# Kernel optimization log

Measured on AMD Instinct MI355X. Metric: run time of the kernel, lower is better.

Reference implementation:

```python
import jax, jax.numpy as jnp
import numpy as np

ANGLE_BITS = 3          # TurboQuantConfig.angle_bits default
LEVELS = 2 ** ANGLE_BITS
PI = np.pi


def _angle_ranges(d_minus_1, dtype):
    # hyperspherical coords: first d-2 angles in [0, pi], last angle in [0, 2*pi)
    return jnp.concatenate([
        jnp.full((d_minus_1 - 1,), PI, dtype),
        jnp.full((1,), 2.0 * PI, dtype),
    ])


def polar_compress(x):
    """x: [..., d] -> (r [...,1], theta_indices int32 [..., d-1])."""
    # suffix norms s_i = ||x[i:]|| via reversed cumsum of squares
    suffix = jnp.sqrt(jnp.cumsum((x * x)[..., ::-1], axis=-1)[..., ::-1])
    r = suffix[..., :1]
    cos_t = jnp.clip(x[..., :-1] / jnp.maximum(suffix[..., :-1], 1e-12), -1.0, 1.0)
    theta = jnp.arccos(cos_t)                      # [..., d-1], in [0, pi]
    # last angle carries the sign of x[..., -1]: map to [0, 2*pi)
    last = jnp.where(x[..., -1:] < 0, 2.0 * PI - theta[..., -1:], theta[..., -1:])
    theta = jnp.concatenate([theta[..., :-1], last], axis=-1)
    ranges = _angle_ranges(theta.shape[-1], theta.dtype)
    idx = jnp.round(theta / ranges * (LEVELS - 1)).astype(jnp.int32)
    return r, idx


def polar_decompress(r, idx):
    """(r [...,1], idx [..., d-1]) -> x_hat [..., d] via trig products."""
    d1 = idx.shape[-1]
    ranges = _angle_ranges(d1, r.dtype)
    theta = idx.astype(r.dtype) / (LEVELS - 1) * ranges
    sinp = jnp.cumprod(jnp.sin(theta), axis=-1)                 # [..., d-1]
    prods = jnp.concatenate([jnp.ones_like(r), sinp], axis=-1)  # [..., d]
    coss = jnp.concatenate([jnp.cos(theta), jnp.ones_like(r)], axis=-1)
    return r * prods * coss


def setup_inputs() -> dict:
    key = jax.random.key(0)
    kq, kk, kv, kn = jax.random.split(key, 4)
    B, H, T, k, d = 1, 32, 8192, 16, 128
    return {
        "queries": jax.random.normal(kq, (B, H, k, d), jnp.float32),
        "keys": jax.random.normal(kk, (B, H, T, d), jnp.float32),
        "values": jax.random.normal(kv, (B, H, T, d), jnp.float32),
        # faithful stand-in for `torch.randn_like(scores) * 0.01` QJL correction,
        # materialized deterministically as an input
        "qjl_noise": jax.random.normal(kn, (B, H, k, T), jnp.float32) * 0.01,
    }


def reference(queries, keys, values, qjl_noise):
    d = queries.shape[-1]
    # compress_kv_cache: polar angle quantization of keys and values
    r_k, idx_k = polar_compress(keys)
    r_v, idx_v = polar_compress(values)
    # compute_attention_with_compressed_kv: decompress-then-attend
    keys_polar = polar_decompress(r_k, idx_k)      # [B,H,T,d]
    values_polar = polar_decompress(r_v, idx_v)    # [B,H,T,d]
    scores = jnp.einsum('bhkd,bhtd->bhkt', queries, keys_polar) / jnp.sqrt(
        jnp.asarray(d, queries.dtype))
    scores = scores + qjl_noise
    attn = jax.nn.softmax(scores, axis=-1)
    return jnp.einsum('bhkt,bhtd->bhkd', attn, values_polar)
```

## Files before the change

### kernel.cpp

```cpp
#include <hip/hip_runtime.h>
#include <math.h>

typedef __attribute__((ext_vector_type(8))) short bf16x8;
typedef __attribute__((ext_vector_type(4))) float f32x4;
typedef __attribute__((ext_vector_type(2))) float f32x2;

#define HEADS 32
#define SEQT  8192
#define DIM   128
#define NQ    16
#define BPH   64
#define BTOK  128
#define WTOK  32
#define CHK   16
#define NPART BPH
#define PSTR  132
#define QSCALE 0.08838834764831845f

#define OFF_QS    0
#define OFF_PS    4096
#define OFF_RAW   8192
#define OFF_KS    24576
#define OFF_ML    0
#define OFF_MERGE 8192
#define LDS_BYTES 40960

#define W1SQ 0.9504844339512096f
#define W2SQ 0.6112604669781572f
#define W3SQ 0.1882550990706332f
#define S1C  0.4338837391175581f
#define S2C  0.7818314824680298f
#define S3C  0.9749279121818236f
#define C1C  0.9009688679024191f
#define C2C  0.6234898018587336f
#define C3C  0.2225209339563144f
#define B1SQ 0.8117449009293667f
#define B2SQ 0.0495155660487913f
#define B3SQ 0.3887395330218429f

#define DPP_QP_XOR1 0xB1
#define DPP_QP_XOR2 0x4E
#define DPP_QP_SHL1 0x39
#define DPP_QP_SHR1 0x90
#define DPP_QP_SHR2 0x44
#define DPP_QP_BC0  0x00
#define DPP_QP_BC3  0xFF
#define DPP_HALF_MIRR 0x141
#define DPP_MIRR      0x140

#define WAITV asm volatile("s_waitcnt vmcnt(0)" ::: "memory")

template <int CTRL>
__device__ __forceinline__ float dpp0(float v) {
  return __int_as_float(__builtin_amdgcn_update_dpp(
      0, __float_as_int(v), CTRL, 0xF, 0xF, true));
}
__device__ __forceinline__ float rmax16(float v) {
  v = fmaxf(v, dpp0<DPP_QP_XOR1>(v));
  v = fmaxf(v, dpp0<DPP_QP_XOR2>(v));
  v = fmaxf(v, dpp0<DPP_HALF_MIRR>(v));
  v = fmaxf(v, dpp0<DPP_MIRR>(v));
  return v;
}
__device__ __forceinline__ float rsum16(float v) {
  v += dpp0<DPP_QP_XOR1>(v);
  v += dpp0<DPP_QP_XOR2>(v);
  v += dpp0<DPP_HALF_MIRR>(v);
  v += dpp0<DPP_MIRR>(v);
  return v;
}
__device__ __forceinline__ float rdlane(float v, int l) {
  return __int_as_float(__builtin_amdgcn_readlane(__float_as_int(v), l));
}
__device__ __forceinline__ unsigned short f2bf(float f) {
  unsigned u = __float_as_uint(f);
  u += 0x7FFFu + ((u >> 16) & 1u);
  return (unsigned short)(u >> 16);
}
__device__ __forceinline__ unsigned cvtpk(float lo, float hi) {
  unsigned r;
  asm("v_cvt_pk_bf16_f32 %0, %1, %2" : "=v"(r) : "v"(lo), "v"(hi));
  return r;
}

__device__ __forceinline__ void stage8(const float* __restrict__ g, char* lds, int lane) {
  const int h2 = lane >> 5;
  const int qs = (lane >> 3) & 3;
  const int js = lane & 7;
#pragma unroll
  for (int i = 0; i < 4; ++i) {
    const int t = 2 * i + h2;
    const int sb = js ^ t;
    __builtin_amdgcn_global_load_lds(
        (const float*)(g + (size_t)t * DIM + qs * 32 + sb * 4),
        (float*)(lds + i * 1024), 16, 0, 0);
  }
}

template <bool KOUT>
__device__ __forceinline__ void decomp8(
    const float* rawW, int lane,
    unsigned short* KsW, float* VsW, int q8,
    const float* nextsrc, char* rawBytes)
{
  const int tloc = lane >> 3;
  const int o    = lane & 7;

  float x[16];
#pragma unroll
  for (int j = 0; j < 4; ++j) {
    const int s = ((o >> 1) << 3) | ((((o & 1) << 2) | j) ^ tloc);
    const float4 v = *(const float4*)(rawW + tloc * 128 + 4 * s);
    x[4*j+0] = v.x; x[4*j+1] = v.y; x[4*j+2] = v.z; x[4*j+3] = v.w;
  }
  asm volatile("s_waitcnt lgkmcnt(0)" ::: "memory");
  __builtin_amdgcn_sched_barrier(0);
  if (nextsrc) stage8(nextsrc, rawBytes, lane);
  __builtin_amdgcn_sched_barrier(0);

  float qa0 = 0.f, qa1 = 0.f;
#pragma unroll
  for (int i = 0; i < 16; i += 2) {
    qa0 = fmaf(x[i], x[i], qa0);
    qa1 = fmaf(x[i+1], x[i+1], qa1);
  }
  const float qs = qa0 + qa1;
  const float a1 = dpp0<DPP_QP_SHL1>(qs);
  const float t1 = qs + (((lane & 3) == 3) ? 0.f : a1);
  const float b1 = dpp0<DPP_QP_XOR2>(t1);
  const float t2 = t1 + (((lane & 3) < 2) ? b1 : 0.f);
  const float qt = dpp0<DPP_QP_BC0>(t2);
  const float ot = dpp0<DPP_HALF_MIRR>(qt);
  const float total = qt + ot;
  const float S = t2 + ((o < 4) ? ot : 0.f);

  const float r = sqrtf(total);

  float run = S, psin = 1.f, run14 = 0.f;
  float sv[16], cv[16];
#pragma unroll
  for (int i = 0; i < 16; ++i) {
    const float u = x[i] * x[i];
    if (i == 14) run14 = run;
    const bool lo2 = u < W2SQ * run;
    const float thr = lo2 ? W3SQ : W1SQ;
    const bool bx = u < thr * run;
    const float ssin = lo2 ? (bx ? S3C : S2C) : (bx ? S1C : 0.f);
    float scos = lo2 ? (bx ? C3C : C2C) : (bx ? C1C : 1.f);
    scos = copysignf(scos, x[i]);
    sv[i] = ssin; cv[i] = scos;
    psin *= ssin;
    run -= u;
  }
  const float p1 = dpp0<DPP_QP_SHR1>(psin);
  const float e1 = psin * (((lane & 3) == 0) ? 1.f : p1);
  const float p2 = dpp0<DPP_QP_SHR2>(e1);
  const float e2 = e1 * (((lane & 3) < 2) ? 1.f : p2);
  const float pq = dpp0<DPP_QP_BC3>(e2);
  const float po = dpp0<DPP_HALF_MIRR>(pq);
  const float e3 = e2 * ((o >= 4) ? po : 1.f);
  const float sh = dpp0<DPP_QP_SHR1>(e3);
  const float E = ((lane & 3) == 0) ? ((o < 4) ? 1.f : po) : sh;

  float rcum = r * E;
  const int T = q8 * 8 + tloc;
#pragma unroll
  for (int g = 0; g < 2; ++g) {
    float outv[8];
    float rc14 = rcum;
#pragma unroll
    for (int k = 0; k < 8; ++k) {
      const int i = 8 * g + k;
      if (i == 14) rc14 = rcum;
      outv[k] = rcum * cv[i];
      rcum *= sv[i];
    }
    if (g == 1) {
      const float u14 = x[14] * x[14];
      const bool neg = x[14] < 0.f;
      const bool cc1 = u14 < B1SQ * run14;
      const bool cc2 = u14 < B2SQ * run14;
      const bool cc3 = u14 > B3SQ * run14;
      const float cpos = cc2 ? -C3C : (cc1 ? C2C : 1.f);
      const float spos = cc2 ? S3C : (cc1 ? S2C : 0.f);
      const float cneg = cc3 ? -C1C : -C3C;
      const float sneg = cc3 ? S1C : S3C;
      const float cB = neg ? cneg : cpos;
      float sB = neg ? sneg : spos;
      sB = copysignf(sB, x[15]);
      const bool o7 = (o == 7);
      outv[6] = o7 ? rc14 * cB : outv[6];
      outv[7] = o7 ? rc14 * sB : outv[7];
    }
    if (KOUT) {
      uint4 w;
      w.x = cvtpk(outv[0], outv[1]);
      w.y = cvtpk(outv[2], outv[3]);
      w.z = cvtpk(outv[4], outv[5]);
      w.w = cvtpk(outv[6], outv[7]);
      *(uint4*)&KsW[T * 128 + ((o * 16 + 8 * g) ^ (tloc << 3))] = w;
    } else {
      const int f0 = (o * 16 + 8 * g) ^ (tloc << 2);
      *(float4*)&VsW[tloc * 128 + f0]       = make_float4(outv[0], outv[1], outv[2], outv[3]);
      *(float4*)&VsW[tloc * 128 + (f0 ^ 4)] = make_float4(outv[4], outv[5], outv[6], outv[7]);
    }
  }
}

__global__ __launch_bounds__(256, 2)
void attn_partial(const float* __restrict__ Q, const float* __restrict__ K,
                  const float* __restrict__ V, const float* __restrict__ noise,
                  float* __restrict__ part) {
  __shared__ __align__(16) char RAW[LDS_BYTES];
  unsigned short* Qs = (unsigned short*)(RAW + OFF_QS);
  float*          Ps = (float*)(RAW + OFF_PS);
  float2*         Ml = (float2*)(RAW + OFF_ML);

  const int tid  = threadIdx.x;
  const int lane = tid & 63;
  const int wv   = tid >> 6;
  const int h    = blockIdx.x / BPH;
  const int bh   = blockIdx.x % BPH;
  const int r16  = lane & 15, G = lane >> 4;

  char* rawB = RAW + OFF_RAW + wv * 4096;
  const float* rawW = (const float*)rawB;
  unsigned short* KsW = (unsigned short*)(RAW + OFF_KS + wv * 4096);
  float* VsW = (float*)KsW;
  float* myP = Ps + wv * (CHK * NQ);

  const size_t hoff = (size_t)h * SEQT * DIM;
  const int t0 = bh * BTOK + wv * WTOK;
  const float* Kg = K + hoff + (size_t)t0 * DIM;
  const float* Vg = V + hoff + (size_t)t0 * DIM;

  stage8(Kg, rawB, lane);
  {
    const float* Qh = Q + (size_t)h * NQ * DIM;
    for (int i = tid; i < NQ * DIM; i += 256)
      Qs[i] = f2bf(Qh[i] * QSCALE);
  }
  __syncthreads();

  bf16x8 qa[4];
#pragma unroll
  for (int c = 0; c < 4; ++c)
    qa[c] = *(const bf16x8*)&Qs[r16 * 128 + c * 32 + G * 8];

  f32x2 acc[NQ];
#pragma unroll
  for (int qq = 0; qq < NQ; ++qq) acc[qq] = (f32x2){0.f, 0.f};
  float m_r[4] = {-INFINITY, -INFINITY, -INFINITY, -INFINITY};
  float l_r[4] = {0.f, 0.f, 0.f, 0.f};

  const float* nh = noise + (size_t)h * NQ * SEQT + t0 + r16;

#pragma unroll 1
  for (int ch = 0; ch < 2; ++ch) {
    const float* KgC = Kg + ch * 2048;
    const float* VgC = Vg + ch * 2048;

    WAITV;
    decomp8<true>(rawW, lane, KsW, VsW, 0, KgC + 1024, rawB);
    WAITV;
    decomp8<true>(rawW, lane, KsW, VsW, 1, VgC, rawB);

    f32x4 d0 = {0.f, 0.f, 0.f, 0.f};
#pragma unroll
    for (int c = 0; c < 4; ++c) {
      bf16x8 b0 = *(const bf16x8*)&KsW[r16 * 128 + ((c * 32 + G * 8) ^ ((r16 & 7) << 3))];
      d0 = __builtin_amdgcn_mfma_f32_16x16x32_bf16(qa[c], b0, d0, 0, 0, 0);
    }
    const float* nt = nh + ch * CHK;
    float s0_[4];
#pragma unroll
    for (int rr = 0; rr < 4; ++rr)
      s0_[rr] = d0[rr] + nt[(size_t)(4 * G + rr) * SEQT];
    float al_r[4];
#pragma unroll
    for (int rr = 0; rr < 4; ++rr) {
      float mt = rmax16(s0_[rr]);
      float mn = fmaxf(m_r[rr], mt);
      al_r[rr] = __expf(m_r[rr] - mn);
      m_r[rr] = mn;
    }
    float p0[4];
#pragma unroll
    for (int rr = 0; rr < 4; ++rr) {
      p0[rr] = __expf(s0_[rr] - m_r[rr]);
      l_r[rr] = l_r[rr] * al_r[rr] + rsum16(p0[rr]);
    }
    *(float4*)&myP[r16 * NQ + 4 * G] = make_float4(p0[0], p0[1], p0[2], p0[3]);
#pragma unroll
    for (int qq = 0; qq < NQ; ++qq) {
      float alq = rdlane(al_r[qq & 3], (qq >> 2) << 4);
      acc[qq] *= (f32x2){alq, alq};
    }

#pragma unroll 1
    for (int sc = 0; sc < 2; ++sc) {
      const float* nxt = (sc == 0) ? (VgC + 1024)
                                   : ((ch == 0) ? (KgC + 2048) : nullptr);
      WAITV;
      decomp8<false>(rawW, lane, KsW, VsW, 0, nxt, rawB);
#pragma unroll 2
      for (int tt = 0; tt < 8; ++tt) {
        float2 vh = *(const float2*)&VsW[tt * 128 + ((2 * lane) ^ (tt << 2))];
        f32x2 vh2 = {vh.x, vh.y};
        const float* pv = &myP[(sc * 8 + tt) * NQ];
        float4 pa = ((const float4*)pv)[0];
        float4 pb = ((const float4*)pv)[1];
        float4 pc = ((const float4*)pv)[2];
        float4 pd = ((const float4*)pv)[3];
        float pq[NQ] = {pa.x, pa.y, pa.z, pa.w, pb.x, pb.y, pb.z, pb.w,
                        pc.x, pc.y, pc.z, pc.w, pd.x, pd.y, pd.z, pd.w};
#pragma unroll
        for (int qq = 0; qq < NQ; ++qq)
          acc[qq] = __builtin_elementwise_fma((f32x2){pq[qq], pq[qq]}, vh2, acc[qq]);
      }
    }
  }

  if (r16 == 0) {
#pragma unroll
    for (int rr = 0; rr < 4; ++rr)
      Ml[wv * NQ + 4 * G + rr] = make_float2(m_r[rr], l_r[rr]);
  }
  __syncthreads();
#pragma unroll
  for (int qq = 0; qq < NQ; ++qq) {
    float2 e0 = Ml[0 * NQ + qq], e1 = Ml[1 * NQ + qq];
    float2 e2 = Ml[2 * NQ + qq], e3 = Ml[3 * NQ + qq];
    float Mq = fmaxf(fmaxf(e0.x, e1.x), fmaxf(e2.x, e3.x));
    float own = (wv == 0) ? e0.x : ((wv == 1) ? e1.x : ((wv == 2) ? e2.x : e3.x));
    float al = __expf(own - Mq);
    acc[qq] *= (f32x2){al, al};
  }
  float* buf = (float*)(RAW + OFF_MERGE);
  if (wv >= 2) {
#pragma unroll
    for (int qq = 0; qq < NQ; ++qq)
      *(float2*)&buf[(wv - 2) * 2048 + qq * 128 + 2 * lane] =
          make_float2(acc[qq].x, acc[qq].y);
  }
  __syncthreads();
  if (wv < 2) {
#pragma unroll
    for (int qq = 0; qq < NQ; ++qq) {
      float2 t = *(const float2*)&buf[wv * 2048 + qq * 128 + 2 * lane];
      acc[qq] += (f32x2){t.x, t.y};
    }
  }
  __syncthreads();
  if (wv == 1) {
#pragma unroll
    for (int qq = 0; qq < NQ; ++qq)
      *(float2*)&buf[qq * 128 + 2 * lane] = make_float2(acc[qq].x, acc[qq].y);
  }
  __syncthreads();
  if (wv == 0) {
    float* P = part + ((size_t)h * NPART + bh) * (NQ * PSTR);
#pragma unroll
    for (int qq = 0; qq < NQ; ++qq) {
      float2 t = *(const float2*)&buf[qq * 128 + 2 * lane];
      *(float2*)&P[qq * PSTR + 4 + 2 * lane] =
          make_float2(acc[qq].x + t.x, acc[qq].y + t.y);
      float2 e0 = Ml[0 * NQ + qq], e1 = Ml[1 * NQ + qq];
      float2 e2 = Ml[2 * NQ + qq], e3 = Ml[3 * NQ + qq];
      float Mq = fmaxf(fmaxf(e0.x, e1.x), fmaxf(e2.x, e3.x));
      float Lq = e0.y * __expf(e0.x - Mq) + e1.y * __expf(e1.x - Mq) +
                 e2.y * __expf(e2.x - Mq) + e3.y * __expf(e3.x - Mq);
      if (lane == 0) *(float2*)&P[qq * PSTR] = make_float2(Mq, Lq);
    }
  }
}

__global__ __launch_bounds__(128)
void attn_reduce(const float* __restrict__ part, float* __restrict__ out) {
  __shared__ float wgt[NPART];
  __shared__ float Lsh;
  const int tid = threadIdx.x;
  const int h = blockIdx.x >> 4;
  const int q = blockIdx.x & 15;
  const float* P = part + (size_t)h * NPART * NQ * PSTR;
  if (tid < NPART) {
    float2 ml = *(const float2*)&P[((size_t)tid * NQ + q) * PSTR];
    float M = ml.x;
#pragma unroll
    for (int off = 1; off < 64; off <<= 1)
      M = fmaxf(M, __shfl_xor(M, off, 64));
    float w = __expf(ml.x - M);
    wgt[tid] = w;
    float L = ml.y * w;
#pragma unroll
    for (int off = 1; off < 64; off <<= 1)
      L += __shfl_xor(L, off, 64);
    if (tid == 0) Lsh = L;
  }
  __syncthreads();
  const float* A = P + (size_t)q * PSTR + 4 + tid;
  float o = 0.f;
#pragma unroll 8
  for (int c = 0; c < NPART; ++c)
    o = fmaf(wgt[c], A[(size_t)c * NQ * PSTR], o);
  out[((size_t)h * NQ + q) * DIM + tid] = o * (1.0f / Lsh);
}

extern "C" void kernel_launch(void* const* d_in, const int* in_sizes, int n_in,
                              void* d_out, int out_size, void* d_ws, size_t ws_size,
                              hipStream_t stream) {
  (void)in_sizes; (void)n_in; (void)out_size; (void)ws_size;
  const float* Q = (const float*)d_in[0];
  const float* K = (const float*)d_in[1];
  const float* V = (const float*)d_in[2];
  const float* noise = (const float*)d_in[3];
  float* part = (float*)d_ws;
  attn_partial<<<dim3(HEADS * BPH), dim3(256), 0, stream>>>(Q, K, V, noise, part);
  attn_reduce<<<dim3(HEADS * NQ), dim3(128), 0, stream>>>(part, (float*)d_out);
}
```

Before: 307.0 us.

## Load raw K/V tiles into registers instead of staging through LDS

Replaces the global_load_lds staging of raw K/V rows, and the swizzled LDS reads that followed, with direct float4 global loads into registers. Double-buffered register arrays (xa/xb) prefetch the next 8-token tile while the current one is decompressed. This drops 16 KB of LDS per block and removes the explicit vmcnt waits and LDS round trips. The cost is 32 more live VGPRs under launch_bounds(256,2), which could cause spills or leave the compiler waiting on loads at first use.

```diff
diff --git a/kernel.cpp b/kernel.cpp
--- a/kernel.cpp
+++ b/kernel.cpp
@@ -19,11 +19,10 @@
 
 #define OFF_QS    0
 #define OFF_PS    4096
-#define OFF_RAW   8192
-#define OFF_KS    24576
+#define OFF_KS    8192
 #define OFF_ML    0
 #define OFF_MERGE 8192
-#define LDS_BYTES 40960
+#define LDS_BYTES 24576
 
 #define W1SQ 0.9504844339512096f
 #define W2SQ 0.6112604669781572f
@@ -48,8 +47,6 @@
 #define DPP_HALF_MIRR 0x141
 #define DPP_MIRR      0x140
 
-#define WAITV asm volatile("s_waitcnt vmcnt(0)" ::: "memory")
-
 template <int CTRL>
 __device__ __forceinline__ float dpp0(float v) {
   return __int_as_float(__builtin_amdgcn_update_dpp(
@@ -83,40 +80,24 @@
   return r;
 }
 
-__device__ __forceinline__ void stage8(const float* __restrict__ g, char* lds, int lane) {
-  const int h2 = lane >> 5;
-  const int qs = (lane >> 3) & 3;
-  const int js = lane & 7;
-#pragma unroll
-  for (int i = 0; i < 4; ++i) {
-    const int t = 2 * i + h2;
-    const int sb = js ^ t;
-    __builtin_amdgcn_global_load_lds(
-        (const float*)(g + (size_t)t * DIM + qs * 32 + sb * 4),
-        (float*)(lds + i * 1024), 16, 0, 0);
-  }
+__device__ __forceinline__ void loadx(float x[16], const float* __restrict__ g, int lane) {
+  const int tloc = lane >> 3;
+  const int o    = lane & 7;
+  const float4* p = (const float4*)(g + tloc * DIM + o * 16);
+  const float4 a = p[0], b = p[1], c = p[2], d = p[3];
+  x[0]=a.x;  x[1]=a.y;  x[2]=a.z;  x[3]=a.w;
+  x[4]=b.x;  x[5]=b.y;  x[6]=b.z;  x[7]=b.w;
+  x[8]=c.x;  x[9]=c.y;  x[10]=c.z; x[11]=c.w;
+  x[12]=d.x; x[13]=d.y; x[14]=d.z; x[15]=d.w;
 }
 
 template <bool KOUT>
 __device__ __forceinline__ void decomp8(
-    const float* rawW, int lane,
-    unsigned short* KsW, float* VsW, int q8,
-    const float* nextsrc, char* rawBytes)
+    const float (&x)[16], int lane,
+    unsigned short* KsW, float* VsW, int q8)
 {
   const int tloc = lane >> 3;
   const int o    = lane & 7;
-
-  float x[16];
-#pragma unroll
-  for (int j = 0; j < 4; ++j) {
-    const int s = ((o >> 1) << 3) | ((((o & 1) << 2) | j) ^ tloc);
-    const float4 v = *(const float4*)(rawW + tloc * 128 + 4 * s);
-    x[4*j+0] = v.x; x[4*j+1] = v.y; x[4*j+2] = v.z; x[4*j+3] = v.w;
-  }
-  asm volatile("s_waitcnt lgkmcnt(0)" ::: "memory");
-  __builtin_amdgcn_sched_barrier(0);
-  if (nextsrc) stage8(nextsrc, rawBytes, lane);
-  __builtin_amdgcn_sched_barrier(0);
 
   float qa0 = 0.f, qa1 = 0.f;
 #pragma unroll
@@ -223,8 +204,6 @@
   const int bh   = blockIdx.x % BPH;
   const int r16  = lane & 15, G = lane >> 4;
 
-  char* rawB = RAW + OFF_RAW + wv * 4096;
-  const float* rawW = (const float*)rawB;
   unsigned short* KsW = (unsigned short*)(RAW + OFF_KS + wv * 4096);
   float* VsW = (float*)KsW;
   float* myP = Ps + wv * (CHK * NQ);
@@ -234,7 +213,8 @@
   const float* Kg = K + hoff + (size_t)t0 * DIM;
   const float* Vg = V + hoff + (size_t)t0 * DIM;
 
-  stage8(Kg, rawB, lane);
+  float xa[16], xb[16];
+  loadx(xa, Kg, lane);
   {
     const float* Qh = Q + (size_t)h * NQ * DIM;
     for (int i = tid; i < NQ * DIM; i += 256)
@@ -260,10 +240,10 @@
     const float* KgC = Kg + ch * 2048;
     const float* VgC = Vg + ch * 2048;
 
-    WAITV;
-    decomp8<true>(rawW, lane, KsW, VsW, 0, KgC + 1024, rawB);
-    WAITV;
-    decomp8<true>(rawW, lane, KsW, VsW, 1, VgC, rawB);
+    loadx(xb, KgC + 1024, lane);
+    decomp8<true>(xa, lane, KsW, VsW, 0);
+    loadx(xa, VgC, lane);
+    decomp8<true>(xb, lane, KsW, VsW, 1);
 
     f32x4 d0 = {0.f, 0.f, 0.f, 0.f};
 #pragma unroll
@@ -297,12 +277,12 @@
       acc[qq] *= (f32x2){alq, alq};
     }
 
+    loadx(xb, VgC + 1024, lane);
 #pragma unroll 1
     for (int sc = 0; sc < 2; ++sc) {
-      const float* nxt = (sc == 0) ? (VgC + 1024)
-                                   : ((ch == 0) ? (KgC + 2048) : nullptr);
-      WAITV;
-      decomp8<false>(rawW, lane, KsW, VsW, 0, nxt, rawB);
+      decomp8<false>(sc == 0 ? xa : xb, lane, KsW, VsW, 0);
+      if (sc == 0 && ch == 0)
+        loadx(xa, KgC + 2048, lane);
 #pragma unroll 2
       for (int tt = 0; tt < 8; ++tt) {
         float2 vh = *(const float2*)&VsW[tt * 128 + ((2 * lane) ^ (tt << 2))];
```

Measured after the change: 309.5 us. Within noise of the previous version (+0.8%).
